# Kernel optimization log

Hardware: AMD Instinct MI355X
Metric: run time of the kernel (lower is better)

Reference implementation:

```python
import jax, jax.numpy as jnp
import numpy as np

NUM_HEADS = 16

def setup_inputs() -> dict:
    key = jax.random.key(0)
    ks = jax.random.split(key, 8)
    T, S, B, E = 2048, 2048, 4, 1024
    s = 0.02
    return {
        "query": jax.random.normal(ks[0], (T, B, E), jnp.float32),
        "key": jax.random.normal(ks[1], (S, B, E), jnp.float32),
        "value": jax.random.normal(ks[2], (S, B, E), jnp.float32),
        "q_proj_weight": jax.random.normal(ks[3], (E, E), jnp.float32) * s,
        "k_proj_weight": jax.random.normal(ks[4], (E, E), jnp.float32) * s,
        "v_proj_weight": jax.random.normal(ks[5], (E, E), jnp.float32) * s,
        "out_proj_weight": jax.random.normal(ks[6], (E, E), jnp.float32) * s,
        "out_proj_bias": jax.random.normal(ks[7], (E,), jnp.float32) * s,
    }

def reference(query, key, value, q_proj_weight, k_proj_weight, v_proj_weight,
              out_proj_weight, out_proj_bias):
    T, B, E = query.shape
    S = key.shape[0]
    H = NUM_HEADS
    hd = E // H
    # F.linear: x @ W.T
    q = jnp.einsum('tbe,fe->tbf', query, q_proj_weight) * (float(hd) ** -0.5)
    k = jnp.einsum('sbe,fe->sbf', key, k_proj_weight)
    v = jnp.einsum('sbe,fe->sbf', value, v_proj_weight)
    # [len, B, E] -> [B*H, len, hd]  (view then transpose, as in torch)
    q = q.reshape(T, B * H, hd).transpose(1, 0, 2)
    k = k.reshape(S, B * H, hd).transpose(1, 0, 2)
    v = v.reshape(S, B * H, hd).transpose(1, 0, 2)
    scores = jnp.einsum('nth,nsh->nts', q, k)      # [B*H, T, S]
    attn = jax.nn.softmax(scores, axis=-1)          # dropout p=0.0 -> identity
    out = jnp.einsum('nts,nsh->nth', attn, v)       # [B*H, T, hd]
    out = out.transpose(1, 0, 2).reshape(T, B, E)
    attn_output = jnp.einsum('tbe,fe->tbf', out, out_proj_weight) + out_proj_bias
    # faithful to original: view(num_heads, batch, T, S) of the [B*H,T,S] buffer
    avg_weights = attn.reshape(H, B, T, S).sum(axis=0) / H  # [B, T, S]
    return attn_output, avg_weights
```

## Files before the change

### kernel.cpp

```cpp
#include <hip/hip_runtime.h>
#include <stdint.h>

#define T_LEN 2048
#define S_LEN 2048
#define BATCH 4
#define EMB 1024
#define NH 16
#define HD 64
#define MROWS 8192

typedef __attribute__((ext_vector_type(8))) __bf16 bfx8;
typedef __attribute__((ext_vector_type(4))) float fx4;
typedef __attribute__((ext_vector_type(16))) float fx16;
typedef __attribute__((ext_vector_type(8))) unsigned short usx8;
typedef __attribute__((ext_vector_type(2))) unsigned int ux2;
typedef __attribute__((ext_vector_type(4))) unsigned int ux4;

typedef __attribute__((address_space(1))) const void GV;
typedef __attribute__((address_space(3))) void LV;
#define GLL(gp, lp) __builtin_amdgcn_global_load_lds((GV*)(gp), (LV*)(lp), 16, 0, 0)

#define QSCALE 0.18033688011112042591f

static __device__ __forceinline__ unsigned short f2bf(float f) {
  unsigned int u = __float_as_uint(f);
  u += 0x7fffu + ((u >> 16) & 1u);
  return (unsigned short)(u >> 16);
}

static __device__ __forceinline__ unsigned int cvt_pk(float lo, float hi) {
  unsigned int r;
  asm("v_cvt_pk_bf16_f32 %0, %1, %2" : "=v"(r) : "v"(lo), "v"(hi));
  return r;
}

static __device__ __forceinline__ void plswap(unsigned int &a, unsigned int &b) {
  auto r = __builtin_amdgcn_permlane32_swap((int)a, (int)b, false, false);
  a = (unsigned int)r[0];
  b = (unsigned int)r[1];
}

#define PIPE_BARRIER(N)                                              \
  do {                                                               \
    asm volatile("s_waitcnt vmcnt(" #N ")" ::: "memory");            \
    __builtin_amdgcn_s_barrier();                                    \
    asm volatile("" ::: "memory");                                   \
  } while (0)

__global__ __launch_bounds__(256) void cast_w(
    const float* __restrict__ wq, const float* __restrict__ wk,
    const float* __restrict__ wv, const float* __restrict__ wo,
    unsigned short* __restrict__ bwq, unsigned short* __restrict__ bwk,
    unsigned short* __restrict__ bwv, unsigned short* __restrict__ bwo)
{
  const long W8 = (long)EMB * EMB / 8;
  long i = (long)blockIdx.x * 256 + threadIdx.x;
  long wch = i / W8, off = i - wch * W8;
  const float* s = (wch == 0) ? wq : (wch == 1) ? wk : (wch == 2) ? wv : wo;
  unsigned short* d = (wch == 0) ? bwq : (wch == 1) ? bwk : (wch == 2) ? bwv : bwo;
  const float4* sp = (const float4*)(s + off * 8);
  float4 a = sp[0], b2 = sp[1];
  usx8 r;
  r[0] = f2bf(a.x);  r[1] = f2bf(a.y);  r[2] = f2bf(a.z);  r[3] = f2bf(a.w);
  r[4] = f2bf(b2.x); r[5] = f2bf(b2.y); r[6] = f2bf(b2.z); r[7] = f2bf(b2.w);
  *(usx8*)(d + off * 8) = r;
}

__global__ __launch_bounds__(256) void qkv_gemm(
    const float* __restrict__ qA, const float* __restrict__ kA, const float* __restrict__ vA,
    const unsigned short* __restrict__ bwq, const unsigned short* __restrict__ bwk,
    const unsigned short* __restrict__ bwv,
    unsigned short* __restrict__ qsb, unsigned short* __restrict__ ksb,
    unsigned short* __restrict__ vtb)
{
  __shared__ unsigned short As[2][128 * 32];
  __shared__ unsigned short Bs[2][128 * 32];
  const int tid = threadIdx.x;
  const int z = blockIdx.z;
  const float* A = (z == 0) ? qA : (z == 1) ? kA : vA;
  const unsigned short* Bw = (z == 0) ? bwq : (z == 1) ? bwk : bwv;
  const int lane = tid & 63;
  const int w = tid >> 6, wr = w >> 1, wc = w & 1;
  const int lr = lane & 15, lhi = lane >> 4;
  const long rowA0 = (long)blockIdx.x * 128;
  const long rowB0 = (long)blockIdx.y * 128;
  fx4 acc[4][4] = {};

  float4 ra[2][2];
  auto loadA = [&](int kt) {
#pragma unroll
    for (int i = 0; i < 2; ++i) {
      int c = tid + i * 256;
      int r = c >> 2, ci = c & 3;
      const float4* p = (const float4*)(A + (rowA0 + r) * 1024 + kt * 32 + ci * 8);
      ra[i][0] = p[0];
      ra[i][1] = p[1];
    }
  };
  auto writeA = [&](int bf) {
#pragma unroll
    for (int i = 0; i < 2; ++i) {
      int c = tid + i * 256;
      int r = c >> 2, ci = c & 3;
      int phys = ci ^ ((r >> 1) & 3);
      ux4 u;
      u.x = cvt_pk(ra[i][0].x, ra[i][0].y);
      u.y = cvt_pk(ra[i][0].z, ra[i][0].w);
      u.z = cvt_pk(ra[i][1].x, ra[i][1].y);
      u.w = cvt_pk(ra[i][1].z, ra[i][1].w);
      *(ux4*)&As[bf][(r * 4 + phys) * 8] = u;
    }
  };
  auto stageB = [&](int kt, int bf) {
#pragma unroll
    for (int i = 0; i < 2; ++i) {
      int c = tid + i * 256;
      int r = c >> 2, ci = c & 3;
      int cs = ci ^ ((r >> 1) & 3);
      GLL(Bw + (rowB0 + r) * 1024 + kt * 32 + cs * 8, &Bs[bf][c * 8]);
    }
  };

  loadA(0);
  stageB(0, 0);
  writeA(0);
  asm volatile("s_waitcnt vmcnt(0) lgkmcnt(0)" ::: "memory");
  __builtin_amdgcn_s_barrier();
  asm volatile("" ::: "memory");

  for (int kt = 0; kt < 32; ++kt) {
    const int bf = kt & 1;
    if (kt < 31) { loadA(kt + 1); stageB(kt + 1, bf ^ 1); }
    bfx8 af[4], bwf[4];
#pragma unroll
    for (int m = 0; m < 4; ++m) {
      int r = wr * 64 + m * 16 + lr;
      af[m] = *(const bfx8*)&As[bf][r * 32 + ((lhi ^ ((r >> 1) & 3)) * 8)];
    }
#pragma unroll
    for (int n = 0; n < 4; ++n) {
      int r = wc * 64 + n * 16 + lr;
      bwf[n] = *(const bfx8*)&Bs[bf][r * 32 + ((lhi ^ ((r >> 1) & 3)) * 8)];
    }
    __builtin_amdgcn_s_setprio(1);
#pragma unroll
    for (int m = 0; m < 4; ++m)
#pragma unroll
      for (int n = 0; n < 4; ++n)
        acc[m][n] = __builtin_amdgcn_mfma_f32_16x16x32_bf16(af[m], bwf[n], acc[m][n], 0, 0, 0);
    __builtin_amdgcn_s_setprio(0);
    if (kt < 31) {
      writeA(bf ^ 1);
      asm volatile("s_waitcnt vmcnt(0) lgkmcnt(0)" ::: "memory");
      __builtin_amdgcn_s_barrier();
      asm volatile("" ::: "memory");
    }
  }
  const float scale = (z == 0) ? QSCALE : 1.0f;
  if (z < 2) {
    unsigned short* out = (z == 0) ? qsb : ksb;
#pragma unroll
    for (int m = 0; m < 4; ++m)
#pragma unroll
      for (int n = 0; n < 4; ++n)
#pragma unroll
        for (int j = 0; j < 4; ++j) {
          long row = rowA0 + wr * 64 + m * 16 + lhi * 4 + j;
          long col = rowB0 + wc * 64 + n * 16 + lr;
          long t = row >> 2, b = row & 3;
          long h = col >> 6, d = col & 63;
          out[((b * 16 + h) * 2048 + t) * 64 + d] = f2bf(acc[m][n][j] * scale);
        }
  } else {
#pragma unroll
    for (int m = 0; m < 4; ++m)
#pragma unroll
      for (int n = 0; n < 4; ++n)
#pragma unroll
        for (int j = 0; j < 4; ++j) {
          long row = rowA0 + wr * 64 + m * 16 + lhi * 4 + j;
          long col = rowB0 + wc * 64 + n * 16 + lr;
          long s = row >> 2, b = row & 3;
          long h = col >> 6, d = col & 63;
          vtb[(((b * 16 + h) * 64 + d) << 11) + s] = f2bf(acc[m][n][j]);
        }
  }
}

__global__ __launch_bounds__(256) void gemm_out(
    const unsigned short* __restrict__ A,
    const unsigned short* __restrict__ Bw,
    float* __restrict__ out,
    const float* __restrict__ bias)
{
  __shared__ unsigned short As[3][128 * 32];
  __shared__ unsigned short Bs[3][128 * 32];
  const int tid = threadIdx.x;
  const int lane = tid & 63;
  const int w = tid >> 6, wr = w >> 1, wc = w & 1;
  const int lr = lane & 15, lhi = lane >> 4;
  const long rowA0 = (long)blockIdx.x * 128;
  const long rowB0 = (long)blockIdx.y * 128;
  fx4 acc[4][4] = {};

  auto stage = [&](int kt, int bf) {
#pragma unroll
    for (int i = 0; i < 2; ++i) {
      int c = tid + i * 256;
      int r = c >> 2, ci = c & 3;
      int cs = ci ^ ((r >> 1) & 3);
      GLL(A + (rowA0 + r) * 1024 + kt * 32 + cs * 8, &As[bf][c * 8]);
      GLL(Bw + (rowB0 + r) * 1024 + kt * 32 + cs * 8, &Bs[bf][c * 8]);
    }
  };

  stage(0, 0);
  stage(1, 1);
  for (int kt = 0; kt < 32; ++kt) {
    const int bf = kt % 3;
    if (kt < 31) PIPE_BARRIER(4); else PIPE_BARRIER(0);
    if (kt + 2 < 32) stage(kt + 2, (kt + 2) % 3);
    bfx8 af[4], bwf[4];
#pragma unroll
    for (int m = 0; m < 4; ++m) {
      int r = wr * 64 + m * 16 + lr;
      af[m] = *(const bfx8*)&As[bf][r * 32 + ((lhi ^ ((r >> 1) & 3)) * 8)];
    }
#pragma unroll
    for (int n = 0; n < 4; ++n) {
      int r = wc * 64 + n * 16 + lr;
      bwf[n] = *(const bfx8*)&Bs[bf][r * 32 + ((lhi ^ ((r >> 1) & 3)) * 8)];
    }
    __builtin_amdgcn_s_setprio(1);
#pragma unroll
    for (int m = 0; m < 4; ++m)
#pragma unroll
      for (int n = 0; n < 4; ++n)
        acc[m][n] = __builtin_amdgcn_mfma_f32_16x16x32_bf16(af[m], bwf[n], acc[m][n], 0, 0, 0);
    __builtin_amdgcn_s_setprio(0);
  }
#pragma unroll
  for (int m = 0; m < 4; ++m)
#pragma unroll
    for (int n = 0; n < 4; ++n)
#pragma unroll
      for (int j = 0; j < 4; ++j) {
        long row = rowA0 + wr * 64 + m * 16 + lhi * 4 + j;
        long col = rowB0 + wc * 64 + n * 16 + lr;
        out[row * 1024 + col] = acc[m][n][j] + bias[col];
      }
}

__global__ __launch_bounds__(512, 4) void flash_fwd(
    const unsigned short* __restrict__ qs, const unsigned short* __restrict__ ks,
    const unsigned short* __restrict__ vt, unsigned short* __restrict__ os,
    float* __restrict__ lgi)
{
  __shared__ unsigned short Kl[3][64 * 64];
  __shared__ unsigned short Vl[3][64 * 64];
  const int tid = threadIdx.x;
  const int w = tid >> 6;
  const int lane = tid & 63;
  const int l31 = lane & 31;
  const int hi = lane >> 5;
  const long bh = blockIdx.x;
  const long t0 = (long)blockIdx.y * 256;
  const unsigned short* kb0 = ks + bh * 2048 * 64;
  const unsigned short* vb0 = vt + bh * 64 * 2048;

  bfx8 qf[4];
  {
    const unsigned short* qp = qs + (bh * 2048 + t0 + w * 32 + l31) * 64;
#pragma unroll
    for (int ksl = 0; ksl < 4; ++ksl)
      qf[ksl] = *(const bfx8*)(qp + ksl * 16 + hi * 8);
  }

  bfx8 ones8;
  {
    union { ux4 u; bfx8 b; } ou;
    ou.u.x = ou.u.y = ou.u.z = ou.u.w = 0x3F803F80u;
    ones8 = ou.b;
  }

  fx16 oacc[2] = {};
  fx16 lacc = {};

  auto stage = [&](int st, int bf) {
    const unsigned short* kp = kb0 + st * 64 * 64;
    const unsigned short* vp = vb0 + st * 64;
    int r = tid >> 3, pc = tid & 7;
    int cs = pc ^ (r & 7);
    GLL(kp + r * 64 + cs * 8, &Kl[bf][tid * 8]);
    GLL(vp + (long)r * 2048 + cs * 8, &Vl[bf][tid * 8]);
  };

  stage(0, 0);
  stage(1, 1);
  for (int st = 0; st < 32; ++st) {
    const int bf = st % 3;
    if (st < 31) PIPE_BARRIER(2); else PIPE_BARRIER(0);
    if (st + 2 < 32) stage(st + 2, (st + 2) % 3);
    fx16 sc[2] = {};
    __builtin_amdgcn_s_setprio(1);
#pragma unroll
    for (int ksl = 0; ksl < 4; ++ksl)
#pragma unroll
      for (int kb = 0; kb < 2; ++kb) {
        int row = kb * 32 + l31;
        int phys = (2 * ksl + hi) ^ (row & 7);
        bfx8 af = *(const bfx8*)&Kl[bf][row * 64 + phys * 8];
        sc[kb] = __builtin_amdgcn_mfma_f32_32x32x16_bf16(af, qf[ksl], sc[kb], 0, 0, 0);
      }
    __builtin_amdgcn_s_setprio(0);
#pragma unroll
    for (int kb = 0; kb < 2; ++kb)
#pragma unroll
      for (int r = 0; r < 16; ++r)
        sc[kb][r] = __builtin_amdgcn_exp2f(sc[kb][r]);
#pragma unroll
    for (int ksl = 0; ksl < 4; ++ksl) {
      const int kb = ksl >> 1;
      const int tb = 2 * (ksl & 1);
      unsigned int A0 = cvt_pk(sc[kb][tb * 4 + 0], sc[kb][tb * 4 + 1]);
      unsigned int A1 = cvt_pk(sc[kb][tb * 4 + 2], sc[kb][tb * 4 + 3]);
      unsigned int B0 = cvt_pk(sc[kb][tb * 4 + 4], sc[kb][tb * 4 + 5]);
      unsigned int B1 = cvt_pk(sc[kb][tb * 4 + 6], sc[kb][tb * 4 + 7]);
      plswap(A0, B0);
      plswap(A1, B1);
      ux4 uw; uw.x = A0; uw.y = A1; uw.z = B0; uw.w = B1;
      union { ux4 u; bfx8 b; } cvv; cvv.u = uw;
      bfx8 pa = cvv.b;
      __builtin_amdgcn_s_setprio(1);
#pragma unroll
      for (int db = 0; db < 2; ++db) {
        int row = db * 32 + l31;
        int phys = (2 * ksl + hi) ^ (row & 7);
        bfx8 vf = *(const bfx8*)&Vl[bf][row * 64 + phys * 8];
        oacc[db] = __builtin_amdgcn_mfma_f32_32x32x16_bf16(vf, pa, oacc[db], 0, 0, 0);
      }
      lacc = __builtin_amdgcn_mfma_f32_32x32x16_bf16(ones8, pa, lacc, 0, 0, 0);
      __builtin_amdgcn_s_setprio(0);
    }
  }
  const long b_ = bh >> 4, h_ = bh & 15;
  {
    float li = 1.f / lacc[0];
    long t = t0 + w * 32 + l31;
    unsigned short* ob = os + (t * 4 + b_) * 1024 + h_ * 64;
#pragma unroll
    for (int db = 0; db < 2; ++db)
#pragma unroll
      for (int tt = 0; tt < 4; ++tt) {
        int d0i = db * 32 + tt * 8 + hi * 4;
        unsigned int u0 = cvt_pk(oacc[db][tt * 4 + 0] * li, oacc[db][tt * 4 + 1] * li);
        unsigned int u1 = cvt_pk(oacc[db][tt * 4 + 2] * li, oacc[db][tt * 4 + 3] * li);
        ux2 uu; uu.x = u0; uu.y = u1;
        *(ux2*)(ob + d0i) = uu;
      }
    if (hi == 0) lgi[bh * 2048 + t] = li;
  }
}

__global__ __launch_bounds__(512, 1) void avg_kernel(
    const unsigned short* __restrict__ qs, const unsigned short* __restrict__ ks,
    const float* __restrict__ lgi, float* __restrict__ avg)
{
  __shared__ unsigned short Qs[2][128 * 64];
  __shared__ unsigned short Ks[2][256 * 64];
  __shared__ float lgl[16 * 128];
  const int tid = threadIdx.x, lane = tid & 63, w = tid >> 6;
  const int l31 = lane & 31, hi = lane >> 5;
  const int wt = w & 3, ws = w >> 2;
  const long b = blockIdx.z;
  const long t0 = (long)blockIdx.x * 128;
  const long s0 = (long)blockIdx.y * 256;
  fx16 aacc[4] = {};

  auto stage = [&](int h, int bf) {
    long bh = b * 16 + h;
    const unsigned short* qb = qs + (bh * 2048 + t0) * 64;
    const unsigned short* kb = ks + (bh * 2048 + s0) * 64;
#pragma unroll
    for (int i = 0; i < 2; ++i) {
      int c = tid + i * 512, r = c >> 3, cs = (c & 7) ^ (r & 7);
      GLL(qb + r * 64 + cs * 8, &Qs[bf][c * 8]);
    }
#pragma unroll
    for (int i = 0; i < 4; ++i) {
      int c = tid + i * 512, r = c >> 3, cs = (c & 7) ^ (r & 7);
      GLL(kb + r * 64 + cs * 8, &Ks[bf][c * 8]);
    }
  };

  GLL(&lgi[(b * 16 + (tid >> 5)) * 2048 + t0 + (tid & 31) * 4], &lgl[tid * 4]);
  stage(0, 0);
  __syncthreads();
  int buf = 0;
  for (int h = 0; h < 16; ++h) {
    if (h < 15) stage(h + 1, buf ^ 1);
    fx16 sacc[4] = {};
    const int arow = wt * 32 + l31;
    __builtin_amdgcn_s_setprio(1);
#pragma unroll
    for (int ksl = 0; ksl < 4; ++ksl) {
      bfx8 aq = *(const bfx8*)&Qs[buf][arow * 64 + (((2 * ksl + hi) ^ (arow & 7)) * 8)];
#pragma unroll
      for (int n = 0; n < 4; ++n) {
        int brow = ws * 128 + n * 32 + l31;
        bfx8 bk = *(const bfx8*)&Ks[buf][brow * 64 + (((2 * ksl + hi) ^ (brow & 7)) * 8)];
        sacc[n] = __builtin_amdgcn_mfma_f32_32x32x16_bf16(aq, bk, sacc[n], 0, 0, 0);
      }
    }
    __builtin_amdgcn_s_setprio(0);
#pragma unroll
    for (int r = 0; r < 16; ++r) {
      float lj = lgl[h * 128 + wt * 32 + (r & 3) + 8 * (r >> 2) + 4 * hi];
#pragma unroll
      for (int n = 0; n < 4; ++n)
        aacc[n][r] += __builtin_amdgcn_exp2f(sacc[n][r]) * lj;
    }
    __syncthreads();
    buf ^= 1;
  }
#pragma unroll
  for (int r = 0; r < 16; ++r) {
    long t = t0 + wt * 32 + (r & 3) + 8 * (r >> 2) + 4 * hi;
#pragma unroll
    for (int n = 0; n < 4; ++n)
      avg[(b * 2048 + t) * 2048 + s0 + ws * 128 + n * 32 + l31] = aacc[n][r] * 0.0625f;
  }
}

extern "C" void kernel_launch(void* const* d_in, const int* in_sizes, int n_in,
                              void* d_out, int out_size, void* d_ws, size_t ws_size,
                              hipStream_t stream)
{
  const float* q   = (const float*)d_in[0];
  const float* k   = (const float*)d_in[1];
  const float* v   = (const float*)d_in[2];
  const float* wq  = (const float*)d_in[3];
  const float* wk  = (const float*)d_in[4];
  const float* wv  = (const float*)d_in[5];
  const float* wo  = (const float*)d_in[6];
  const float* bias= (const float*)d_in[7];
  char* ws = (char*)d_ws;
  const long MB = 1024 * 1024;
  unsigned short* bwq = (unsigned short*)(ws + 0 * MB);
  unsigned short* bwk = (unsigned short*)(ws + 2 * MB);
  unsigned short* bwv = (unsigned short*)(ws + 4 * MB);
  unsigned short* bwo = (unsigned short*)(ws + 6 * MB);
  unsigned short* qsb = (unsigned short*)(ws + 56 * MB);
  unsigned short* ksb = (unsigned short*)(ws + 72 * MB);
  unsigned short* vtb = (unsigned short*)(ws + 104 * MB);
  unsigned short* osb = (unsigned short*)(ws + 120 * MB);
  float* lgi = (float*)(ws + 137 * MB);
  float* outp = (float*)d_out;

  cast_w<<<2048, 256, 0, stream>>>(wq, wk, wv, wo, bwq, bwk, bwv, bwo);
  qkv_gemm<<<dim3(64, 8, 3), 256, 0, stream>>>(q, k, v, bwq, bwk, bwv, qsb, ksb, vtb);
  flash_fwd<<<dim3(64, 8), 512, 0, stream>>>(qsb, ksb, vtb, osb, lgi);
  avg_kernel<<<dim3(16, 8, 4), 512, 0, stream>>>(qsb, ksb, lgi, outp + 8388608);
  gemm_out<<<dim3(64, 8), 256, 0, stream>>>(osb, bwo, (float*)d_out, bias);
}
```

Baseline: 287.5 us.

## Give each flash wave two query tiles and compute row sums with VALU

```diff
diff --git a/kernel.cpp b/kernel.cpp
--- a/kernel.cpp
+++ b/kernel.cpp
@@ -38,6 +38,12 @@
   auto r = __builtin_amdgcn_permlane32_swap((int)a, (int)b, false, false);
   a = (unsigned int)r[0];
   b = (unsigned int)r[1];
+}
+
+static __device__ __forceinline__ float xhalf_sum(float x) {
+  unsigned int a = __float_as_uint(x), b = a;
+  plswap(a, b);
+  return __uint_as_float(a) + __uint_as_float(b);
 }
 
 #define PIPE_BARRIER(N)                                              \
@@ -251,7 +257,7 @@
       }
 }
 
-__global__ __launch_bounds__(512, 4) void flash_fwd(
+__global__ __launch_bounds__(256, 3) void flash_fwd(
     const unsigned short* __restrict__ qs, const unsigned short* __restrict__ ks,
     const unsigned short* __restrict__ vt, unsigned short* __restrict__ os,
     float* __restrict__ lgi)
@@ -268,40 +274,40 @@
   const unsigned short* kb0 = ks + bh * 2048 * 64;
   const unsigned short* vb0 = vt + bh * 64 * 2048;
 
-  bfx8 qf[4];
+  bfx8 qf[2][4];
   {
-    const unsigned short* qp = qs + (bh * 2048 + t0 + w * 32 + l31) * 64;
-#pragma unroll
-    for (int ksl = 0; ksl < 4; ++ksl)
-      qf[ksl] = *(const bfx8*)(qp + ksl * 16 + hi * 8);
-  }
-
-  bfx8 ones8;
-  {
-    union { ux4 u; bfx8 b; } ou;
-    ou.u.x = ou.u.y = ou.u.z = ou.u.w = 0x3F803F80u;
-    ones8 = ou.b;
-  }
-
-  fx16 oacc[2] = {};
-  fx16 lacc = {};
+    const unsigned short* qp = qs + (bh * 2048 + t0 + w * 64 + l31) * 64;
+#pragma unroll
+    for (int qb = 0; qb < 2; ++qb)
+#pragma unroll
+      for (int ksl = 0; ksl < 4; ++ksl)
+        qf[qb][ksl] = *(const bfx8*)(qp + qb * 32 * 64 + ksl * 16 + hi * 8);
+  }
+
+  fx16 oacc[2][2] = {};
+  fx4 lp0 = {0.f, 0.f, 0.f, 0.f};
+  fx4 lp1 = {0.f, 0.f, 0.f, 0.f};
 
   auto stage = [&](int st, int bf) {
     const unsigned short* kp = kb0 + st * 64 * 64;
     const unsigned short* vp = vb0 + st * 64;
-    int r = tid >> 3, pc = tid & 7;
-    int cs = pc ^ (r & 7);
-    GLL(kp + r * 64 + cs * 8, &Kl[bf][tid * 8]);
-    GLL(vp + (long)r * 2048 + cs * 8, &Vl[bf][tid * 8]);
+#pragma unroll
+    for (int i = 0; i < 2; ++i) {
+      int c = tid + i * 256;
+      int r = c >> 3, pc = c & 7;
+      int cs = pc ^ (r & 7);
+      GLL(kp + r * 64 + cs * 8, &Kl[bf][c * 8]);
+      GLL(vp + (long)r * 2048 + cs * 8, &Vl[bf][c * 8]);
+    }
   };
 
   stage(0, 0);
   stage(1, 1);
   for (int st = 0; st < 32; ++st) {
     const int bf = st % 3;
-    if (st < 31) PIPE_BARRIER(2); else PIPE_BARRIER(0);
+    if (st < 31) PIPE_BARRIER(4); else PIPE_BARRIER(0);
     if (st + 2 < 32) stage(st + 2, (st + 2) % 3);
-    fx16 sc[2] = {};
+    fx16 sc[2][2] = {};
     __builtin_amdgcn_s_setprio(1);
 #pragma unroll
     for (int ksl = 0; ksl < 4; ++ksl)
@@ -310,51 +316,73 @@
         int row = kb * 32 + l31;
         int phys = (2 * ksl + hi) ^ (row & 7);
         bfx8 af = *(const bfx8*)&Kl[bf][row * 64 + phys * 8];
-        sc[kb] = __builtin_amdgcn_mfma_f32_32x32x16_bf16(af, qf[ksl], sc[kb], 0, 0, 0);
+        sc[0][kb] = __builtin_amdgcn_mfma_f32_32x32x16_bf16(af, qf[0][ksl], sc[0][kb], 0, 0, 0);
+        sc[1][kb] = __builtin_amdgcn_mfma_f32_32x32x16_bf16(af, qf[1][ksl], sc[1][kb], 0, 0, 0);
       }
     __builtin_amdgcn_s_setprio(0);
 #pragma unroll
     for (int kb = 0; kb < 2; ++kb)
 #pragma unroll
-      for (int r = 0; r < 16; ++r)
-        sc[kb][r] = __builtin_amdgcn_exp2f(sc[kb][r]);
+      for (int r = 0; r < 16; ++r) {
+        float p0 = __builtin_amdgcn_exp2f(sc[0][kb][r]);
+        float p1 = __builtin_amdgcn_exp2f(sc[1][kb][r]);
+        sc[0][kb][r] = p0;
+        sc[1][kb][r] = p1;
+        lp0[r & 3] += p0;
+        lp1[r & 3] += p1;
+      }
 #pragma unroll
     for (int ksl = 0; ksl < 4; ++ksl) {
       const int kb = ksl >> 1;
       const int tb = 2 * (ksl & 1);
-      unsigned int A0 = cvt_pk(sc[kb][tb * 4 + 0], sc[kb][tb * 4 + 1]);
-      unsigned int A1 = cvt_pk(sc[kb][tb * 4 + 2], sc[kb][tb * 4 + 3]);
-      unsigned int B0 = cvt_pk(sc[kb][tb * 4 + 4], sc[kb][tb * 4 + 5]);
-      unsigned int B1 = cvt_pk(sc[kb][tb * 4 + 6], sc[kb][tb * 4 + 7]);
-      plswap(A0, B0);
-      plswap(A1, B1);
-      ux4 uw; uw.x = A0; uw.y = A1; uw.z = B0; uw.w = B1;
-      union { ux4 u; bfx8 b; } cvv; cvv.u = uw;
-      bfx8 pa = cvv.b;
+      bfx8 pa0, pa1;
+      {
+        unsigned int A0 = cvt_pk(sc[0][kb][tb * 4 + 0], sc[0][kb][tb * 4 + 1]);
+        unsigned int A1 = cvt_pk(sc[0][kb][tb * 4 + 2], sc[0][kb][tb * 4 + 3]);
+        unsigned int B0 = cvt_pk(sc[0][kb][tb * 4 + 4], sc[0][kb][tb * 4 + 5]);
+        unsigned int B1 = cvt_pk(sc[0][kb][tb * 4 + 6], sc[0][kb][tb * 4 + 7]);
+        plswap(A0, B0);
+        plswap(A1, B1);
+        ux4 uw; uw.x = A0; uw.y = A1; uw.z = B0; uw.w = B1;
+        union { ux4 u; bfx8 b; } cvv; cvv.u = uw; pa0 = cvv.b;
+      }
+      {
+        unsigned int A0 = cvt_pk(sc[1][kb][tb * 4 + 0], sc[1][kb][tb * 4 + 1]);
+        unsigned int A1 = cvt_pk(sc[1][kb][tb * 4 + 2], sc[1][kb][tb * 4 + 3]);
+        unsigned int B0 = cvt_pk(sc[1][kb][tb * 4 + 4], sc[1][kb][tb * 4 + 5]);
+        unsigned int B1 = cvt_pk(sc[1][kb][tb * 4 + 6], sc[1][kb][tb * 4 + 7]);
+        plswap(A0, B0);
+        plswap(A1, B1);
+        ux4 uw; uw.x = A0; uw.y = A1; uw.z = B0; uw.w = B1;
+        union { ux4 u; bfx8 b; } cvv; cvv.u = uw; pa1 = cvv.b;
+      }
       __builtin_amdgcn_s_setprio(1);
 #pragma unroll
       for (int db = 0; db < 2; ++db) {
         int row = db * 32 + l31;
         int phys = (2 * ksl + hi) ^ (row & 7);
         bfx8 vf = *(const bfx8*)&Vl[bf][row * 64 + phys * 8];
-        oacc[db] = __builtin_amdgcn_mfma_f32_32x32x16_bf16(vf, pa, oacc[db], 0, 0, 0);
-      }
-      lacc = __builtin_amdgcn_mfma_f32_32x32x16_bf16(ones8, pa, lacc, 0, 0, 0);
+        oacc[0][db] = __builtin_amdgcn_mfma_f32_32x32x16_bf16(vf, pa0, oacc[0][db], 0, 0, 0);
+        oacc[1][db] = __builtin_amdgcn_mfma_f32_32x32x16_bf16(vf, pa1, oacc[1][db], 0, 0, 0);
+      }
       __builtin_amdgcn_s_setprio(0);
     }
   }
   const long b_ = bh >> 4, h_ = bh & 15;
-  {
-    float li = 1.f / lacc[0];
-    long t = t0 + w * 32 + l31;
+  float l0 = xhalf_sum((lp0[0] + lp0[1]) + (lp0[2] + lp0[3]));
+  float l1 = xhalf_sum((lp1[0] + lp1[1]) + (lp1[2] + lp1[3]));
+#pragma unroll
+  for (int qb = 0; qb < 2; ++qb) {
+    float li = 1.f / (qb ? l1 : l0);
+    long t = t0 + w * 64 + qb * 32 + l31;
     unsigned short* ob = os + (t * 4 + b_) * 1024 + h_ * 64;
 #pragma unroll
     for (int db = 0; db < 2; ++db)
 #pragma unroll
       for (int tt = 0; tt < 4; ++tt) {
         int d0i = db * 32 + tt * 8 + hi * 4;
-        unsigned int u0 = cvt_pk(oacc[db][tt * 4 + 0] * li, oacc[db][tt * 4 + 1] * li);
-        unsigned int u1 = cvt_pk(oacc[db][tt * 4 + 2] * li, oacc[db][tt * 4 + 3] * li);
+        unsigned int u0 = cvt_pk(oacc[qb][db][tt * 4 + 0] * li, oacc[qb][db][tt * 4 + 1] * li);
+        unsigned int u1 = cvt_pk(oacc[qb][db][tt * 4 + 2] * li, oacc[qb][db][tt * 4 + 3] * li);
         ux2 uu; uu.x = u0; uu.y = u1;
         *(ux2*)(ob + d0i) = uu;
       }
@@ -459,7 +487,7 @@
 
   cast_w<<<2048, 256, 0, stream>>>(wq, wk, wv, wo, bwq, bwk, bwv, bwo);
   qkv_gemm<<<dim3(64, 8, 3), 256, 0, stream>>>(q, k, v, bwq, bwk, bwv, qsb, ksb, vtb);
-  flash_fwd<<<dim3(64, 8), 512, 0, stream>>>(qsb, ksb, vtb, osb, lgi);
+  flash_fwd<<<dim3(64, 8), 256, 0, stream>>>(qsb, ksb, vtb, osb, lgi);
   avg_kernel<<<dim3(16, 8, 4), 512, 0, stream>>>(qsb, ksb, lgi, outp + 8388608);
   gemm_out<<<dim3(64, 8), 256, 0, stream>>>(osb, bwo, (float*)d_out, bias);
 }
```

New measurement: 327.8 us. 1.14x slower.
